# Performance work log

Hardware: AMD Instinct MI355X
Metric: run time of the kernel (lower is better)

The kernel has to match this reference:

```python
import jax, jax.numpy as jnp
import numpy as np

N, K, FC, FX, E = 16384, 16, 2, 32, 256


def _lin_init(key, fin, fout):
    kw, kb = jax.random.split(key)
    s = 1.0 / np.sqrt(fin)
    W = jax.random.uniform(kw, (fin, fout), jnp.float32, -s, s)
    b = jax.random.uniform(kb, (fout,), jnp.float32, -s, s)
    return W, b


def setup_inputs() -> dict:
    key = jax.random.key(0)
    ks = jax.random.split(key, 13)
    c = jax.random.uniform(ks[0], (N, FC), jnp.float32)
    x = jax.random.normal(ks[1], (N, FX), jnp.float32)
    W_coords, b_coords = _lin_init(ks[2], FC, E)
    W_attri, b_attri = _lin_init(ks[3], FX, E)
    W_g1, b_g1 = _lin_init(ks[4], FC, E)
    W_g2, b_g2 = _lin_init(ks[5], E, E)
    W_g3, b_g3 = _lin_init(ks[6], E, E)
    W_f1, b_f1 = _lin_init(ks[7], FX, E)
    W_f2, b_f2 = _lin_init(ks[8], E, E)
    W_f3, b_f3 = _lin_init(ks[9], E, E)
    W_d1, b_d1 = _lin_init(ks[10], 2 * E, 2 * E)
    W_d2, b_d2 = _lin_init(ks[11], 2 * E, 2)
    return dict(c=c, x=x,
                W_coords=W_coords, b_coords=b_coords,
                W_attri=W_attri, b_attri=b_attri,
                W_g1=W_g1, b_g1=b_g1, W_g2=W_g2, b_g2=b_g2, W_g3=W_g3, b_g3=b_g3,
                W_f1=W_f1, b_f1=b_f1, W_f2=W_f2, b_f2=b_f2, W_f3=W_f3, b_f3=b_f3,
                W_d1=W_d1, b_d1=b_d1, W_d2=W_d2, b_d2=b_d2)


def knn_edges(c, k):
    # PyG knn_graph (loop=False, flow='source_to_target'):
    # edge_index[0]=neighbor(src), edge_index[1]=node(dst).
    n = c.shape[0]
    sq = jnp.sum(c * c, axis=1)
    d2 = sq[:, None] + sq[None, :] - 2.0 * (c @ c.T)  # [N,N] squared dists
    d2 = d2.at[jnp.arange(n), jnp.arange(n)].set(jnp.inf)  # exclude self
    _, idx = jax.lax.top_k(-d2, k)  # [N,k] nearest neighbor indices
    src = idx.reshape(-1)
    dst = jnp.repeat(jnp.arange(n), k)
    return src, dst


def gcn_conv(h, src, dst, ew, W, b):
    # PyG GCNConv: linear -> add self-loops (weight 1) -> sym norm -> scatter-add -> +bias
    n = h.shape[0]
    hw = h @ W
    loop = jnp.arange(n)
    s = jnp.concatenate([src, loop])
    d = jnp.concatenate([dst, loop])
    w = jnp.concatenate([ew, jnp.ones((n,), h.dtype)])
    deg = jax.ops.segment_sum(w, d, num_segments=n)
    dinv = jnp.where(deg > 0, jax.lax.rsqrt(deg), 0.0)
    norm = dinv[s] * w * dinv[d]
    out = jax.ops.segment_sum(norm[:, None] * hw[s], d, num_segments=n)
    return out + b


def reference(c, x, W_coords, b_coords, W_attri, b_attri,
              W_g1, b_g1, W_g2, b_g2, W_g3, b_g3,
              W_f1, b_f1, W_f2, b_f2, W_f3, b_f3,
              W_d1, b_d1, W_d2, b_d2):
    src, dst = knn_edges(c, K)
    dist = jnp.linalg.norm(c[src] - c[dst], axis=1)
    ew = jnp.exp(-dist / 2.0)
    ew = jnp.where(ew > 10.0, 0.0, ew)  # faithful to source (never triggers)

    coords0 = c @ W_coords + b_coords
    attri0 = x @ W_attri + b_attri

    # eval mode: dropout is identity
    g1 = jax.nn.relu(gcn_conv(c, src, dst, ew, W_g1, b_g1))
    m1 = jax.nn.relu(x @ W_f1 + b_f1)
    g1 = coords0 + g1
    m1 = attri0 + m1

    g2 = jax.nn.relu(gcn_conv(g1, src, dst, ew, W_g2, b_g2))
    m2 = jax.nn.relu(m1 @ W_f2 + b_f2)
    g2 = g1 + g2
    m2 = m1 + m2

    g3 = jax.nn.relu(gcn_conv(g2, src, dst, ew, W_g3, b_g3))
    m3 = jax.nn.relu(m2 @ W_f3 + b_f3)
    g3 = g2 + g3
    m3 = m2 + m3

    combined = jnp.concatenate([g3, m3], axis=1)
    out = jax.nn.relu(combined @ W_d1 + b_d1) @ W_d2 + b_d2
    mean = out[:, 0]
    sigma = 0.2 + 0.8 * jax.nn.softplus(out[:, 1])
    return mean.reshape(-1, 1), sigma.reshape(-1, 1), g3, m3
```

## Files before the change

### kernel.cpp

```cpp
#include <hip/hip_runtime.h>
#include <math.h>

#define NPTS 16384
#define KNN 16
#define GRES 128
#define NCELL (GRES * GRES)
#define CAP 16

typedef unsigned long long ull;
typedef __attribute__((ext_vector_type(8))) short  bf16x8;
typedef __attribute__((ext_vector_type(4))) float  f32x4;

__device__ inline unsigned short f2bf(float f) {
    unsigned int u = __float_as_uint(f);
    u += 0x7fffu + ((u >> 16) & 1u);
    return (unsigned short)(u >> 16);
}
__device__ inline float bf2f(unsigned short u) {
    return __uint_as_float(((unsigned int)u) << 16);
}

__global__ __launch_bounds__(256) void wprep_kernel(
    const float* __restrict__ W0, const float* __restrict__ W1,
    const float* __restrict__ W2, const float* __restrict__ W3,
    const float* __restrict__ W4,
    unsigned short* __restrict__ D0, unsigned short* __restrict__ D1,
    unsigned short* __restrict__ D2, unsigned short* __restrict__ D3,
    unsigned short* __restrict__ D4, int* __restrict__ cnt)
{
    const int z = blockIdx.z;
    if (z == 5) {
        const int i = (blockIdx.y * 16 + blockIdx.x) * 256 + threadIdx.x;
        if (i < NCELL) cnt[i] = 0;
        return;
    }
    const float* W; unsigned short* D; int K;
    if (z == 0) { W = W0; D = D0; K = 256; }
    else if (z == 1) { W = W1; D = D1; K = 256; }
    else if (z == 2) { W = W2; D = D2; K = 256; }
    else if (z == 3) { W = W3; D = D3; K = 256; }
    else { W = W4; D = D4; K = 512; }
    const int nt = K / 32;
    if (blockIdx.x >= nt || blockIdx.y >= nt) return;
    const int k0 = blockIdx.x * 32, n0 = blockIdx.y * 32;
    __shared__ float t[32][33];
    const int tr = threadIdx.x >> 5, tc = threadIdx.x & 31;
#pragma unroll
    for (int i = 0; i < 4; ++i)
        t[tr + i * 8][tc] = W[(size_t)(k0 + tr + i * 8) * K + n0 + tc];
    __syncthreads();
#pragma unroll
    for (int i = 0; i < 4; ++i)
        D[(size_t)(n0 + tr + i * 8) * K + k0 + tc] = f2bf(t[tc][tr + i * 8]);
}

__global__ __launch_bounds__(256) void count_scatter_kernel(const float2* __restrict__ c,
    int* __restrict__ cnt, float4* __restrict__ pts)
{
    const int i = blockIdx.x * 256 + threadIdx.x;
    float2 p = c[i];
    int cx = min(GRES - 1, max(0, (int)(p.x * GRES)));
    int cy = min(GRES - 1, max(0, (int)(p.y * GRES)));
    int cell = cy * GRES + cx;
    int slot = atomicAdd(&cnt[cell], 1);
    if (slot < CAP) {
        float4 v;
        v.x = p.x; v.y = p.y; v.z = __uint_as_float((unsigned int)i); v.w = 0.f;
        pts[cell * CAP + slot] = v;
    }
}

__global__ __launch_bounds__(256) void knn_query_kernel(const float2* __restrict__ c,
    const float4* __restrict__ pts, const int* __restrict__ cnt,
    int* __restrict__ nbr, float* __restrict__ ew, float* __restrict__ dinv)
{
    const int lane = threadIdx.x & 63;
    const int qidx = blockIdx.x * 4 + (threadIdx.x >> 6);
    const float2 qc = c[qidx];
    const float qx = qc.x, qy = qc.y;
    const int qcx = min(GRES - 1, max(0, (int)(qx * GRES)));
    const int qcy = min(GRES - 1, max(0, (int)(qy * GRES)));

    ull cur = ~0ULL;

    auto process = [&](int ccy, int ccx, bool valid) {
        int s0 = 0, len = 0;
        if (valid && ccy >= 0 && ccy < GRES && ccx >= 0 && ccx < GRES) {
            const int cell = ccy * GRES + ccx;
            s0 = cell * CAP;
            len = min(cnt[cell], CAP);
        }
        int pin = len;
#pragma unroll
        for (int off = 1; off < 64; off <<= 1) {
            int v = __shfl_up(pin, off, 64);
            pin += (lane >= off) ? v : 0;
        }
        const int T = __shfl(pin, 63, 64);
        const int pex = pin - len;
        for (int b = 0; b < T; b += 64) {
            const int ci = b + lane;
            const int cq = min(ci, T - 1);
            int lo = 0, hi = 63;
#pragma unroll
            for (int it = 0; it < 6; ++it) {
                const int mid = (lo + hi) >> 1;
                const int pm = __shfl(pin, mid, 64);
                if (pm > cq) hi = mid; else lo = mid + 1;
            }
            const int cs = __shfl(s0, hi, 64);
            const int cb = __shfl(pex, hi, 64);
            const int p  = cs + (cq - cb);
            const float4 pp = pts[p];
            const float dx = pp.x - qx, dy = pp.y - qy;
            const float d2 = fmaf(dx, dx, dy * dy);
            const int pidx = (int)__float_as_uint(pp.z);
            ull key = ~0ULL;
            if (ci < T && pidx != qidx)
                key = (((ull)__float_as_uint(d2)) << 32) | (ull)__float_as_uint(pp.z);
#pragma unroll
            for (int k = 2; k <= 64; k <<= 1) {
#pragma unroll
                for (int j = k >> 1; j > 0; j >>= 1) {
                    ull o = __shfl_xor(key, j, 64);
                    bool takeMin = (((lane & k) == 0) == ((lane & j) == 0));
                    ull mn = (o < key) ? o : key;
                    ull mx = (o > key) ? o : key;
                    key = takeMin ? mn : mx;
                }
            }
            ull rev = __shfl(key, (31 - lane) & 63, 64);
            ull val = (lane < 16) ? cur : ((lane < 32) ? rev : ~0ULL);
#pragma unroll
            for (int j = 16; j > 0; j >>= 1) {
                ull o = __shfl_xor(val, j, 64);
                ull mn = (o < val) ? o : val;
                ull mx = (o > val) ? o : val;
                val = ((lane & j) == 0) ? mn : mx;
            }
            cur = (lane < 16) ? val : ~0ULL;
        }
    };

    process(qcy - 3 + lane / 7, qcx - 3 + (lane % 7), lane < 49);

    int R = 3;
    const float h = 1.0f / GRES;
    while (true) {
        ull k15 = __shfl(cur, 15, 64);
        float dmax = __uint_as_float((unsigned int)(k15 >> 32));
        float rr = 0.999f * (float)R * h;
        if (dmax < rr * rr) break;
        if (R >= GRES) break;
        ++R;
        const int ncells = 8 * R;
        for (int cc = 0; cc < ncells; cc += 64) {
            const int i = cc + lane;
            int ccy = 0, ccx = 0;
            const bool valid = (i < ncells);
            if (valid) {
                const int side = 2 * R + 1;
                if (i < side)            { ccy = qcy - R; ccx = qcx - R + i; }
                else if (i < 2 * side)   { ccy = qcy + R; ccx = qcx - R + (i - side); }
                else {
                    const int j = i - 2 * side;
                    ccy = qcy - R + 1 + (j >> 1);
                    ccx = (j & 1) ? (qcx + R) : (qcx - R);
                }
            }
            process(ccy, ccx, valid);
        }
    }

    float w = 0.f; int nb = 0;
    if (lane < 16) {
        nb = (int)(cur & 0xffffffffu);
        float d2 = __uint_as_float((unsigned int)(cur >> 32));
        w = expf(-0.5f * sqrtf(d2));
    }
    float acc = w;
#pragma unroll
    for (int off = 1; off < 64; off <<= 1) acc += __shfl_xor(acc, off, 64);
    if (lane < 16) {
        nbr[qidx * KNN + lane] = nb;
        ew[qidx * KNN + lane]  = w;
    }
    if (lane == 0) dinv[qidx] = 1.0f / sqrtf(1.0f + acc);
}

__global__ __launch_bounds__(256) void init_fused_kernel(
    const float* __restrict__ x, const float2* __restrict__ c,
    const int* __restrict__ nbr, const float* __restrict__ ew, const float* __restrict__ dinv,
    const float* __restrict__ Wa, const float* __restrict__ ba,
    const float* __restrict__ Wf, const float* __restrict__ bf,
    const float* __restrict__ Wc, const float* __restrict__ bc,
    const float* __restrict__ Wg, const float* __restrict__ bg,
    float* __restrict__ m1f, unsigned short* __restrict__ m1b,
    float* __restrict__ g1f, unsigned short* __restrict__ g1b)
{
    __shared__ float smem[64 * 32];
    const int tid = threadIdx.x;
    if (blockIdx.x < 256) {
        const int i0 = blockIdx.x * 64;
#pragma unroll
        for (int it = 0; it < 8; ++it)
            smem[tid + it * 256] = x[(size_t)i0 * 32 + tid + it * 256];
        float wa[32], wf[32];
#pragma unroll
        for (int k = 0; k < 32; ++k) { wa[k] = Wa[k * 256 + tid]; wf[k] = Wf[k * 256 + tid]; }
        const float b0 = ba[tid], b1 = bf[tid];
        __syncthreads();
        for (int r = 0; r < 64; ++r) {
            float a0 = b0, a1 = b1;
#pragma unroll
            for (int k = 0; k < 32; ++k) {
                float xv = smem[r * 32 + k];
                a0 = fmaf(xv, wa[k], a0);
                a1 = fmaf(xv, wf[k], a1);
            }
            const float v = a0 + fmaxf(a1, 0.0f);
            m1f[(size_t)(i0 + r) * 256 + tid] = v;
            m1b[(size_t)(i0 + r) * 256 + tid] = f2bf(v);
        }
    } else {
        float (*su)[5] = (float(*)[5])smem;
        const int i0 = (blockIdx.x - 256) * 64;
        if (tid < 64) {
            const int i = i0 + tid;
            float ux = 0.f, uy = 0.f;
            for (int t = 0; t < KNN; ++t) {
                int nb = nbr[i * KNN + t];
                float w = ew[i * KNN + t] * dinv[nb];
                float2 cn = c[nb];
                ux = fmaf(w, cn.x, ux); uy = fmaf(w, cn.y, uy);
            }
            float di = dinv[i];
            float2 ci = c[i];
            ux = fmaf(di, ci.x, ux); uy = fmaf(di, ci.y, uy);
            su[tid][0] = ux; su[tid][1] = uy; su[tid][2] = ci.x; su[tid][3] = ci.y; su[tid][4] = di;
        }
        __syncthreads();
        const float wc0 = Wc[tid], wc1 = Wc[256 + tid];
        const float wg0 = Wg[tid], wg1 = Wg[256 + tid];
        const float bcj = bc[tid], bgj = bg[tid];
        for (int r = 0; r < 64; ++r) {
            float ux = su[r][0], uy = su[r][1], cx = su[r][2], cy = su[r][3], di = su[r][4];
            float coords0 = fmaf(cx, wc0, fmaf(cy, wc1, bcj));
            float pre = fmaf(di, fmaf(ux, wg0, uy * wg1), bgj);
            const float v = coords0 + fmaxf(pre, 0.0f);
            g1f[(size_t)(i0 + r) * 256 + tid] = v;
            g1b[(size_t)(i0 + r) * 256 + tid] = f2bf(v);
        }
    }
}

__global__ __launch_bounds__(256) void agg_kernel(const unsigned short* __restrict__ hw,
    const int* __restrict__ nbr, const float* __restrict__ ew, const float* __restrict__ dinv,
    const float* __restrict__ bias, const float* __restrict__ res,
    float* __restrict__ outf, unsigned short* __restrict__ outb)
{
    __shared__ int   sn[16][16];
    __shared__ float sw[16][16];
    __shared__ float sdi[16];
    const int tid = threadIdx.x;
    const int i0  = blockIdx.x * 16;
    {
        const int r = tid >> 4, t = tid & 15;
        const int i = i0 + r;
        int nb = nbr[i * KNN + t];
        sn[r][t] = nb;
        sw[r][t] = ew[i * KNN + t] * dinv[nb];
        if (t == 0) sdi[r] = dinv[i];
    }
    __syncthreads();
    const float bj = bias[tid];
    for (int r = 0; r < 16; ++r) {
        const int i = i0 + r;
        const float di = sdi[r];
        float s = di * bf2f(hw[(size_t)i * 256 + tid]);
#pragma unroll
        for (int t = 0; t < KNN; ++t)
            s = fmaf(sw[r][t], bf2f(hw[(size_t)sn[r][t] * 256 + tid]), s);
        float v = fmaf(di, s, bj);
        v = res[(size_t)i * 256 + tid] + fmaxf(v, 0.0f);
        outf[(size_t)i * 256 + tid] = v;
        outb[(size_t)i * 256 + tid] = f2bf(v);
    }
}

struct GemmOp {
    const unsigned short *A1, *A2; int ksplit;
    const unsigned short *Wt; int ncols, Kdim;
    const float *bias; const float *res;
    float *outf; unsigned short *outb;
    const float *Wd2; float *part;
    int flags;
};
#define GL 40
__global__ __launch_bounds__(256) void gemm_bf16_kernel(GemmOp opA, GemmOp opB)
{
    const GemmOp op = (blockIdx.z == 0) ? opA : opB;
    __shared__ unsigned short As[128 * GL];
    __shared__ unsigned short Bs[128 * GL];
    const int tid = threadIdx.x;
    const int r0 = blockIdx.x * 128;
    const int c0 = blockIdx.y * 128;
    const int w  = tid >> 6;
    const int wr = w >> 1, wc = w & 1;
    const int l  = tid & 63;
    const int half = l >> 4, lc = l & 15;

    const int srow = tid >> 2;
    const int skq  = (tid & 3) * 8;

    f32x4 acc[4][4];
#pragma unroll
    for (int mt = 0; mt < 4; ++mt)
#pragma unroll
        for (int nt = 0; nt < 4; ++nt) acc[mt][nt] = (f32x4){0.f, 0.f, 0.f, 0.f};

    for (int k0 = 0; k0 < op.Kdim; k0 += 32) {
        const unsigned short* Asrc = (k0 < op.ksplit) ? (op.A1 + k0) : (op.A2 + (k0 - op.ksplit));
#pragma unroll
        for (int it = 0; it < 2; ++it) {
            const int r = srow + it * 64;
            *(bf16x8*)&As[r * GL + skq] = *(const bf16x8*)(Asrc + (size_t)(r0 + r) * 256 + skq);
        }
#pragma unroll
        for (int it = 0; it < 2; ++it) {
            const int n = srow + it * 64;
            *(bf16x8*)&Bs[n * GL + skq] = *(const bf16x8*)(op.Wt + (size_t)(c0 + n) * op.Kdim + k0 + skq);
        }
        __syncthreads();
        bf16x8 af[4], bq[4];
#pragma unroll
        for (int mt = 0; mt < 4; ++mt)
            af[mt] = *(const bf16x8*)&As[(wr * 64 + mt * 16 + lc) * GL + half * 8];
#pragma unroll
        for (int nt = 0; nt < 4; ++nt)
            bq[nt] = *(const bf16x8*)&Bs[(wc * 64 + nt * 16 + lc) * GL + half * 8];
#pragma unroll
        for (int mt = 0; mt < 4; ++mt)
#pragma unroll
            for (int nt = 0; nt < 4; ++nt)
                acc[mt][nt] = __builtin_amdgcn_mfma_f32_16x16x32_bf16(af[mt], bq[nt], acc[mt][nt], 0, 0, 0);
        __syncthreads();
    }

    if (op.flags & 32) {
        float p0[4][4], p1[4][4];
#pragma unroll
        for (int mt = 0; mt < 4; ++mt)
#pragma unroll
            for (int r = 0; r < 4; ++r) { p0[mt][r] = 0.f; p1[mt][r] = 0.f; }
#pragma unroll
        for (int nt = 0; nt < 4; ++nt) {
            const int col = c0 + wc * 64 + nt * 16 + lc;
            const float bv = op.bias[col];
            const float w0 = op.Wd2[col * 2 + 0];
            const float w1 = op.Wd2[col * 2 + 1];
#pragma unroll
            for (int mt = 0; mt < 4; ++mt)
#pragma unroll
                for (int r = 0; r < 4; ++r) {
                    float v = fmaxf(acc[mt][nt][r] + bv, 0.f);
                    p0[mt][r] = fmaf(v, w0, p0[mt][r]);
                    p1[mt][r] = fmaf(v, w1, p1[mt][r]);
                }
        }
#pragma unroll
        for (int mt = 0; mt < 4; ++mt)
#pragma unroll
            for (int r = 0; r < 4; ++r) {
#pragma unroll
                for (int j = 1; j < 16; j <<= 1) {
                    p0[mt][r] += __shfl_xor(p0[mt][r], j, 64);
                    p1[mt][r] += __shfl_xor(p1[mt][r], j, 64);
                }
            }
        if (lc == 0) {
            float* part = op.part + ((size_t)blockIdx.y * 2 + wc) * NPTS * 2;
#pragma unroll
            for (int mt = 0; mt < 4; ++mt) {
                const int rowb = r0 + wr * 64 + mt * 16 + half * 4;
#pragma unroll
                for (int r = 0; r < 4; ++r) {
                    part[(size_t)(rowb + r) * 2 + 0] = p0[mt][r];
                    part[(size_t)(rowb + r) * 2 + 1] = p1[mt][r];
                }
            }
        }
        return;
    }
#pragma unroll
    for (int nt = 0; nt < 4; ++nt) {
        const int col = c0 + wc * 64 + nt * 16 + lc;
        const float bv = (op.flags & 1) ? op.bias[col] : 0.f;
#pragma unroll
        for (int mt = 0; mt < 4; ++mt) {
            const int rowb = r0 + wr * 64 + mt * 16 + half * 4;
#pragma unroll
            for (int r = 0; r < 4; ++r) {
                float v = acc[mt][nt][r] + bv;
                if (op.flags & 2) v = fmaxf(v, 0.f);
                if (op.flags & 4) v += op.res[(size_t)(rowb + r) * op.ncols + col];
                if (op.flags & 8)  op.outf[(size_t)(rowb + r) * op.ncols + col] = v;
                if (op.flags & 16) op.outb[(size_t)(rowb + r) * op.ncols + col] = f2bf(v);
            }
        }
    }
}

__global__ __launch_bounds__(256) void finish_kernel(const float* __restrict__ part,
    const float* __restrict__ b, float* __restrict__ mean, float* __restrict__ sigma)
{
    const int i = blockIdx.x * 256 + threadIdx.x;
    float a0 = 0.f, a1 = 0.f;
#pragma unroll
    for (int j = 0; j < 8; ++j) {
        a0 += part[(size_t)j * NPTS * 2 + 2 * i];
        a1 += part[(size_t)j * NPTS * 2 + 2 * i + 1];
    }
    mean[i] = a0 + b[0];
    float z = a1 + b[1];
    float sp = fmaxf(z, 0.f) + log1pf(expf(-fabsf(z)));
    sigma[i] = fmaf(0.8f, sp, 0.2f);
}

extern "C" void kernel_launch(void* const* d_in, const int* in_sizes, int n_in,
                              void* d_out, int out_size, void* d_ws, size_t ws_size,
                              hipStream_t stream)
{
    (void)in_sizes; (void)n_in; (void)out_size; (void)ws_size;
    const float* c   = (const float*)d_in[0];
    const float* x   = (const float*)d_in[1];
    const float* Wc  = (const float*)d_in[2];
    const float* bc  = (const float*)d_in[3];
    const float* Wa  = (const float*)d_in[4];
    const float* ba  = (const float*)d_in[5];
    const float* Wg1 = (const float*)d_in[6];
    const float* bg1 = (const float*)d_in[7];
    const float* Wg2 = (const float*)d_in[8];
    const float* bg2 = (const float*)d_in[9];
    const float* Wg3 = (const float*)d_in[10];
    const float* bg3 = (const float*)d_in[11];
    const float* Wf1 = (const float*)d_in[12];
    const float* bf1 = (const float*)d_in[13];
    const float* Wf2 = (const float*)d_in[14];
    const float* bf2 = (const float*)d_in[15];
    const float* Wf3 = (const float*)d_in[16];
    const float* bf3 = (const float*)d_in[17];
    const float* Wd1 = (const float*)d_in[18];
    const float* bd1 = (const float*)d_in[19];
    const float* Wd2 = (const float*)d_in[20];
    const float* bd2 = (const float*)d_in[21];

    float* out = (float*)d_out;
    const size_t N = NPTS;
    const size_t SLOT = N * 256;
    float* wsf  = (float*)d_ws;
    int*   nbr  = (int*)d_ws;
    float* ew   = wsf + N * 16;
    float* dinv = wsf + N * 32;
    float* s0   = wsf + N * 33;
    float* s1   = s0 + SLOT;
    float* s2   = s1 + SLOT;
    unsigned short* b0 = (unsigned short*)(s2 + SLOT);
    unsigned short* b1 = b0 + SLOT;
    unsigned short* b2 = b1 + SLOT;
    unsigned short* b3 = b2 + SLOT;
    unsigned short* wb = b3 + SLOT;
    unsigned short* bWg2 = wb;
    unsigned short* bWf2 = wb + 65536;
    unsigned short* bWg3 = wb + 131072;
    unsigned short* bWf3 = wb + 196608;
    unsigned short* bWd1 = wb + 262144;
    float* part = (float*)(wb + 262144 + 262144);

    float4* g_pts  = (float4*)s2;
    int* g_cnt     = (int*)(s2 + (size_t)NCELL * CAP * 4);

    float* o_mean  = out;
    float* o_sigma = out + N;
    float* o_g3    = out + 2 * N;
    float* o_m3    = out + 2 * N + N * 256;

    wprep_kernel<<<dim3(16, 16, 6), 256, 0, stream>>>(Wg2, Wf2, Wg3, Wf3, Wd1,
                                                      bWg2, bWf2, bWg3, bWf3, bWd1, g_cnt);
    count_scatter_kernel<<<NPTS / 256, 256, 0, stream>>>((const float2*)c, g_cnt, g_pts);
    knn_query_kernel<<<NPTS / 4, 256, 0, stream>>>((const float2*)c, g_pts, g_cnt, nbr, ew, dinv);
    init_fused_kernel<<<512, 256, 0, stream>>>(x, (const float2*)c, nbr, ew, dinv,
                                               Wa, ba, Wf1, bf1, Wc, bc, Wg1, bg1,
                                               s0, b0, s1, b1);

    GemmOp z{};
    GemmOp ohw2 = z; ohw2.A1 = b1; ohw2.A2 = b1; ohw2.ksplit = 256; ohw2.Wt = bWg2;
    ohw2.ncols = 256; ohw2.Kdim = 256; ohw2.outb = b2; ohw2.flags = 16;
    GemmOp om2 = z; om2.A1 = b0; om2.A2 = b0; om2.ksplit = 256; om2.Wt = bWf2;
    om2.ncols = 256; om2.Kdim = 256; om2.bias = bf2; om2.res = s0;
    om2.outf = s2; om2.outb = b3; om2.flags = 31;
    gemm_bf16_kernel<<<dim3(NPTS / 128, 2, 2), 256, 0, stream>>>(ohw2, om2);
    agg_kernel<<<1024, 256, 0, stream>>>(b2, nbr, ew, dinv, bg2, s1, s1, b1);

    GemmOp ohw3 = z; ohw3.A1 = b1; ohw3.A2 = b1; ohw3.ksplit = 256; ohw3.Wt = bWg3;
    ohw3.ncols = 256; ohw3.Kdim = 256; ohw3.outb = b2; ohw3.flags = 16;
    GemmOp om3 = z; om3.A1 = b3; om3.A2 = b3; om3.ksplit = 256; om3.Wt = bWf3;
    om3.ncols = 256; om3.Kdim = 256; om3.bias = bf3; om3.res = s2;
    om3.outf = o_m3; om3.outb = b0; om3.flags = 31;
    gemm_bf16_kernel<<<dim3(NPTS / 128, 2, 2), 256, 0, stream>>>(ohw3, om3);
    agg_kernel<<<1024, 256, 0, stream>>>(b2, nbr, ew, dinv, bg3, s1, o_g3, b1);

    GemmOp oh = z; oh.A1 = b1; oh.A2 = b0; oh.ksplit = 256; oh.Wt = bWd1;
    oh.ncols = 512; oh.Kdim = 512; oh.bias = bd1; oh.Wd2 = Wd2; oh.part = part;
    oh.flags = 32;
    gemm_bf16_kernel<<<dim3(NPTS / 128, 4, 1), 256, 0, stream>>>(oh, oh);
    finish_kernel<<<NPTS / 256, 256, 0, stream>>>(part, bd2, o_mean, o_sigma);
}
```

Before: 289.4 us.

## Double-buffer GEMM tiles via global_load_lds with swizzle; vectorize GCN aggregation

The bf16 MFMA GEMM now stages 64-wide K tiles straight from global memory into two LDS buffers using global_load_lds. It uses an XOR swizzle to avoid bank conflicts, and it prefetches the next tile while computing the current one. This is meant to hide load latency and remove the register round-trip and one barrier per step. Separately, the aggregation kernel handles 8 rows per block, with each thread doing 8 contiguous columns through 16-byte loads and stores instead of scalar accesses. The GEMM pipeline relies on correct wait handling for the asynchronous LDS loads, and larger LDS use may lower occupancy.

```diff
diff --git a/kernel.cpp b/kernel.cpp
--- a/kernel.cpp
+++ b/kernel.cpp
@@ -18,6 +18,11 @@
 }
 __device__ inline float bf2f(unsigned short u) {
     return __uint_as_float(((unsigned int)u) << 16);
+}
+
+__device__ inline void glds16(const void* g, void* l) {
+    __builtin_amdgcn_global_load_lds((const __attribute__((address_space(1))) void*)g,
+                                     (__attribute__((address_space(3))) void*)l, 16, 0, 0);
 }
 
 __global__ __launch_bounds__(256) void wprep_kernel(
@@ -259,33 +264,53 @@
     const float* __restrict__ bias, const float* __restrict__ res,
     float* __restrict__ outf, unsigned short* __restrict__ outb)
 {
-    __shared__ int   sn[16][16];
-    __shared__ float sw[16][16];
-    __shared__ float sdi[16];
+    __shared__ int   sn[8][16];
+    __shared__ float sw[8][16];
+    __shared__ float sdi[8];
     const int tid = threadIdx.x;
-    const int i0  = blockIdx.x * 16;
-    {
+    const int i0  = blockIdx.x * 8;
+    if (tid < 128) {
         const int r = tid >> 4, t = tid & 15;
         const int i = i0 + r;
-        int nb = nbr[i * KNN + t];
+        const int nb = nbr[i * KNN + t];
         sn[r][t] = nb;
         sw[r][t] = ew[i * KNN + t] * dinv[nb];
         if (t == 0) sdi[r] = dinv[i];
     }
     __syncthreads();
-    const float bj = bias[tid];
-    for (int r = 0; r < 16; ++r) {
-        const int i = i0 + r;
-        const float di = sdi[r];
-        float s = di * bf2f(hw[(size_t)i * 256 + tid]);
-#pragma unroll
-        for (int t = 0; t < KNN; ++t)
-            s = fmaf(sw[r][t], bf2f(hw[(size_t)sn[r][t] * 256 + tid]), s);
-        float v = fmaf(di, s, bj);
-        v = res[(size_t)i * 256 + tid] + fmaxf(v, 0.0f);
-        outf[(size_t)i * 256 + tid] = v;
-        outb[(size_t)i * 256 + tid] = f2bf(v);
-    }
+    const int rl = tid >> 5;
+    const int c0 = (tid & 31) * 8;
+    const int i  = i0 + rl;
+    const float di = sdi[rl];
+    float acc[8];
+    {
+        const bf16x8 h = *(const bf16x8*)&hw[(size_t)i * 256 + c0];
+#pragma unroll
+        for (int e = 0; e < 8; ++e) acc[e] = di * bf2f((unsigned short)h[e]);
+    }
+#pragma unroll
+    for (int t = 0; t < KNN; ++t) {
+        const float w = sw[rl][t];
+        const bf16x8 h = *(const bf16x8*)&hw[(size_t)sn[rl][t] * 256 + c0];
+#pragma unroll
+        for (int e = 0; e < 8; ++e) acc[e] = fmaf(w, bf2f((unsigned short)h[e]), acc[e]);
+    }
+    float bb[8], rv[8], vo[8];
+    *(float4*)&bb[0] = *(const float4*)&bias[c0];
+    *(float4*)&bb[4] = *(const float4*)&bias[c0 + 4];
+    *(float4*)&rv[0] = *(const float4*)&res[(size_t)i * 256 + c0];
+    *(float4*)&rv[4] = *(const float4*)&res[(size_t)i * 256 + c0 + 4];
+    bf16x8 ob;
+#pragma unroll
+    for (int e = 0; e < 8; ++e) {
+        float v = fmaf(di, acc[e], bb[e]);
+        v = rv[e] + fmaxf(v, 0.0f);
+        vo[e] = v;
+        ob[e] = (short)f2bf(v);
+    }
+    *(float4*)&outf[(size_t)i * 256 + c0]     = *(const float4*)&vo[0];
+    *(float4*)&outf[(size_t)i * 256 + c0 + 4] = *(const float4*)&vo[4];
+    *(bf16x8*)&outb[(size_t)i * 256 + c0] = ob;
 }
 
 struct GemmOp {
@@ -296,12 +321,11 @@
     const float *Wd2; float *part;
     int flags;
 };
-#define GL 40
 __global__ __launch_bounds__(256) void gemm_bf16_kernel(GemmOp opA, GemmOp opB)
 {
     const GemmOp op = (blockIdx.z == 0) ? opA : opB;
-    __shared__ unsigned short As[128 * GL];
-    __shared__ unsigned short Bs[128 * GL];
+    __shared__ unsigned short As[2][128 * 64];
+    __shared__ unsigned short Bs[2][128 * 64];
     const int tid = threadIdx.x;
     const int r0 = blockIdx.x * 128;
     const int c0 = blockIdx.y * 128;
@@ -310,41 +334,57 @@
     const int l  = tid & 63;
     const int half = l >> 4, lc = l & 15;
 
-    const int srow = tid >> 2;
-    const int skq  = (tid & 3) * 8;
-
     f32x4 acc[4][4];
 #pragma unroll
     for (int mt = 0; mt < 4; ++mt)
 #pragma unroll
         for (int nt = 0; nt < 4; ++nt) acc[mt][nt] = (f32x4){0.f, 0.f, 0.f, 0.f};
 
-    for (int k0 = 0; k0 < op.Kdim; k0 += 32) {
+    auto stage = [&](int b, int k0) {
         const unsigned short* Asrc = (k0 < op.ksplit) ? (op.A1 + k0) : (op.A2 + (k0 - op.ksplit));
-#pragma unroll
-        for (int it = 0; it < 2; ++it) {
-            const int r = srow + it * 64;
-            *(bf16x8*)&As[r * GL + skq] = *(const bf16x8*)(Asrc + (size_t)(r0 + r) * 256 + skq);
-        }
-#pragma unroll
-        for (int it = 0; it < 2; ++it) {
-            const int n = srow + it * 64;
-            *(bf16x8*)&Bs[n * GL + skq] = *(const bf16x8*)(op.Wt + (size_t)(c0 + n) * op.Kdim + k0 + skq);
-        }
-        __syncthreads();
-        bf16x8 af[4], bq[4];
-#pragma unroll
-        for (int mt = 0; mt < 4; ++mt)
-            af[mt] = *(const bf16x8*)&As[(wr * 64 + mt * 16 + lc) * GL + half * 8];
-#pragma unroll
-        for (int nt = 0; nt < 4; ++nt)
-            bq[nt] = *(const bf16x8*)&Bs[(wc * 64 + nt * 16 + lc) * GL + half * 8];
-#pragma unroll
-        for (int mt = 0; mt < 4; ++mt)
-#pragma unroll
-            for (int nt = 0; nt < 4; ++nt)
-                acc[mt][nt] = __builtin_amdgcn_mfma_f32_16x16x32_bf16(af[mt], bq[nt], acc[mt][nt], 0, 0, 0);
-        __syncthreads();
+        const unsigned short* Bsrc = op.Wt + k0;
+#pragma unroll
+        for (int it = 0; it < 4; ++it) {
+            const int g = tid + it * 256;
+            const int r = g >> 3;
+            const int s = (g & 7) ^ (r & 7);
+            glds16(Asrc + (size_t)(r0 + r) * 256 + s * 8, &As[b][g * 8]);
+        }
+#pragma unroll
+        for (int it = 0; it < 4; ++it) {
+            const int g = tid + it * 256;
+            const int r = g >> 3;
+            const int s = (g & 7) ^ (r & 7);
+            glds16(Bsrc + (size_t)(c0 + r) * op.Kdim + s * 8, &Bs[b][g * 8]);
+        }
+    };
+
+    const int NT = op.Kdim >> 6;
+    stage(0, 0);
+    __syncthreads();
+    int cur = 0;
+    for (int t = 0; t < NT; ++t) {
+        if (t + 1 < NT) stage(cur ^ 1, (t + 1) << 6);
+#pragma unroll
+        for (int ks = 0; ks < 2; ++ks) {
+            bf16x8 af[4], bq[4];
+#pragma unroll
+            for (int mt = 0; mt < 4; ++mt) {
+                const int rr = wr * 64 + mt * 16 + lc;
+                af[mt] = *(const bf16x8*)&As[cur][rr * 64 + ((((ks << 2) + half) ^ (rr & 7)) << 3)];
+            }
+#pragma unroll
+            for (int nt = 0; nt < 4; ++nt) {
+                const int rr = wc * 64 + nt * 16 + lc;
+                bq[nt] = *(const bf16x8*)&Bs[cur][rr * 64 + ((((ks << 2) + half) ^ (rr & 7)) << 3)];
+            }
+#pragma unroll
+            for (int mt = 0; mt < 4; ++mt)
+#pragma unroll
+                for (int nt = 0; nt < 4; ++nt)
+                    acc[mt][nt] = __builtin_amdgcn_mfma_f32_16x16x32_bf16(af[mt], bq[nt], acc[mt][nt], 0, 0, 0);
+        }
+        if (t + 1 < NT) { __syncthreads(); cur ^= 1; }
     }
 
     if (op.flags & 32) {
@@ -500,7 +540,7 @@
     om2.ncols = 256; om2.Kdim = 256; om2.bias = bf2; om2.res = s0;
     om2.outf = s2; om2.outb = b3; om2.flags = 31;
     gemm_bf16_kernel<<<dim3(NPTS / 128, 2, 2), 256, 0, stream>>>(ohw2, om2);
-    agg_kernel<<<1024, 256, 0, stream>>>(b2, nbr, ew, dinv, bg2, s1, s1, b1);
+    agg_kernel<<<NPTS / 8, 256, 0, stream>>>(b2, nbr, ew, dinv, bg2, s1, s1, b1);
 
     GemmOp ohw3 = z; ohw3.A1 = b1; ohw3.A2 = b1; ohw3.ksplit = 256; ohw3.Wt = bWg3;
     ohw3.ncols = 256; ohw3.Kdim = 256; ohw3.outb = b2; ohw3.flags = 16;
@@ -508,7 +548,7 @@
     om3.ncols = 256; om3.Kdim = 256; om3.bias = bf3; om3.res = s2;
     om3.outf = o_m3; om3.outb = b0; om3.flags = 31;
     gemm_bf16_kernel<<<dim3(NPTS / 128, 2, 2), 256, 0, stream>>>(ohw3, om3);
-    agg_kernel<<<1024, 256, 0, stream>>>(b2, nbr, ew, dinv, bg3, s1, o_g3, b1);
+    agg_kernel<<<NPTS / 8, 256, 0, stream>>>(b2, nbr, ew, dinv, bg3, s1, o_g3, b1);
 
     GemmOp oh = z; oh.A1 = b1; oh.A2 = b0; oh.ksplit = 256; oh.Wt = bWd1;
     oh.ncols = 512; oh.Kdim = 512; oh.bias = bd1; oh.Wd2 = Wd2; oh.part = part;
```

New measurement: 275.4 us. -4.8%, faster.
